# Performance work log

Hardware: AMD Instinct MI355X
Metric: run time of the kernel (lower is better)

Reference implementation:

```python
import jax, jax.numpy as jnp
import numpy as np

N_BINS = 15


def setup_inputs() -> dict:
    key = jax.random.key(0)
    k1, k2 = jax.random.split(key)
    N, C = 1000000, 100
    logits = jax.random.normal(k1, (N, C), dtype=jnp.float32)
    labels = jax.random.randint(k2, (N,), 0, C, dtype=jnp.int64)
    return {"logits": logits, "labels": labels, "t_opt": 0}


def reference(logits, labels, t_opt):
    # temperature scaling branch (t_opt is a static Python int)
    scaled = logits / t_opt if t_opt != 0 else logits
    probs = jax.nn.softmax(scaled, axis=-1)            # [N, C]
    confidences = jnp.max(probs, axis=1)               # [N]
    predictions = jnp.argmax(probs, axis=1)            # [N]
    accuracies = (predictions == labels).astype(jnp.float32)

    # bin index: confidences in (bin_lower, bin_upper] -> single-pass histogram
    boundaries = jnp.linspace(0.0, 1.0, N_BINS + 1)
    bin_idx = jnp.clip(
        jnp.searchsorted(boundaries, confidences, side="left") - 1, 0, N_BINS - 1
    )

    ones = jnp.ones_like(confidences)
    counts = jax.ops.segment_sum(ones, bin_idx, num_segments=N_BINS)
    sum_conf = jax.ops.segment_sum(confidences, bin_idx, num_segments=N_BINS)
    sum_acc = jax.ops.segment_sum(accuracies, bin_idx, num_segments=N_BINS)

    n = confidences.shape[0]
    safe = jnp.maximum(counts, 1.0)
    avg_conf = sum_conf / safe
    avg_acc = sum_acc / safe
    prop = counts / n
    per_bin = jnp.where(counts > 0, jnp.abs(avg_conf - avg_acc) * prop, 0.0)
    return jnp.sum(per_bin).reshape(1)
```

## Files before the change

kernel.cpp:

```cpp
#include <hip/hip_runtime.h>
#include <math.h>

#define NBINS 15
#define TILE_ROWS 128
#define NC 100
#define BLOCK 256
#define TILE_BYTES (TILE_ROWS * NC * 4)
#define CHUNKS (TILE_BYTES / 1024)

typedef __attribute__((address_space(3))) unsigned int lds_u32;
typedef __attribute__((address_space(1))) const unsigned int glob_u32;

__global__ __launch_bounds__(BLOCK, 3) void ece_main(const float* __restrict__ logits,
                                                     const int* __restrict__ labels,
                                                     const int* __restrict__ t_opt,
                                                     float* __restrict__ gbins,
                                                     int N) {
    __shared__ float s_tile[TILE_ROWS * NC];
    __shared__ float s_cnt[NBINS], s_conf[NBINS], s_acc[NBINS];

    const int tid  = threadIdx.x;
    if (tid < NBINS) { s_cnt[tid] = 0.f; s_conf[tid] = 0.f; s_acc[tid] = 0.f; }

    const int lane = tid & 63;
    const int wv   = tid >> 6;
    const int r    = tid >> 1;
    const int h    = tid & 1;

    const int t = t_opt[0];
    const float scale = (t != 0) ? (1.0f / (float)t) : 1.0f;
    const int nTiles = (N + TILE_ROWS - 1) / TILE_ROWS;

    for (int tile = blockIdx.x; tile < nTiles; tile += gridDim.x) {
        const long long base = (long long)tile * TILE_ROWS;
        const int rowsHere  = min(TILE_ROWS, (int)(N - base));
        const int bytesHere = rowsHere * (NC * 4);
        const char* gsrc = (const char*)(logits + base * NC);

        __syncthreads();

        #pragma unroll
        for (int i = 0; i < 13; ++i) {
            const int c = wv + i * 4;
            if (c < CHUNKS) {
                const int off = c * 1024 + lane * 16;
                if (off < bytesHere) {
                    __builtin_amdgcn_global_load_lds(
                        (glob_u32*)(gsrc + off),
                        (lds_u32*)((char*)s_tile + c * 1024),
                        16, 0, 0);
                }
            }
        }
        __syncthreads();

        if (base + r < N) {
            const float4* rowp = (const float4*)&s_tile[r * NC];
            const int n4 = 13 - h;

            float4 v[13];
            #pragma unroll
            for (int j = 0; j < 13; ++j)
                if (j < n4) v[j] = rowp[h * 13 + j];

            float m = -INFINITY; int mi = 0;
            #pragma unroll
            for (int j = 0; j < 13; ++j) if (j < n4) {
                const int cb = (h * 13 + j) * 4;
                float4 w = v[j];
                w.x *= scale; w.y *= scale; w.z *= scale; w.w *= scale;
                v[j] = w;
                if (w.x > m) { m = w.x; mi = cb;     }
                if (w.y > m) { m = w.y; mi = cb + 1; }
                if (w.z > m) { m = w.z; mi = cb + 2; }
                if (w.w > m) { m = w.w; mi = cb + 3; }
            }
            const float om  = __shfl_xor(m, 1);
            const int   omi = __shfl_xor(mi, 1);
            if (om > m || (om == m && omi < mi)) { m = om; mi = omi; }

            float e = 0.f;
            #pragma unroll
            for (int j = 0; j < 13; ++j) if (j < n4) {
                const float4 w = v[j];
                e += __expf(w.x - m) + __expf(w.y - m)
                   + __expf(w.z - m) + __expf(w.w - m);
            }
            e += __shfl_xor(e, 1);

            if (h == 0) {
                const float conf = 1.0f / e;
                const float acc  = (mi == labels[base + r]) ? 1.0f : 0.0f;

                int jc = 0;
                #pragma unroll
                for (int i = 0; i <= NBINS; ++i) {
                    const float b = (float)i * (1.0f / 15.0f);
                    jc += (b < conf) ? 1 : 0;
                }
                int bin = jc - 1;
                bin = bin < 0 ? 0 : (bin > NBINS - 1 ? NBINS - 1 : bin);

                atomicAdd(&s_cnt[bin],  1.0f);
                atomicAdd(&s_conf[bin], conf);
                atomicAdd(&s_acc[bin],  acc);
            }
        }
    }

    __syncthreads();
    if (tid < NBINS) {
        atomicAdd(&gbins[tid],             s_cnt[tid]);
        atomicAdd(&gbins[NBINS + tid],     s_conf[tid]);
        atomicAdd(&gbins[2 * NBINS + tid], s_acc[tid]);
    }
}

__global__ void ece_final(const float* __restrict__ gbins,
                          float* __restrict__ out, int N) {
    if (threadIdx.x == 0 && blockIdx.x == 0) {
        float ece = 0.f;
        for (int b = 0; b < NBINS; ++b) {
            const float c = gbins[b];
            if (c > 0.f) {
                const float avg_conf = gbins[NBINS + b] / c;
                const float avg_acc  = gbins[2 * NBINS + b] / c;
                ece += fabsf(avg_conf - avg_acc) * (c / (float)N);
            }
        }
        out[0] = ece;
    }
}

extern "C" void kernel_launch(void* const* d_in, const int* in_sizes, int n_in,
                              void* d_out, int out_size, void* d_ws, size_t ws_size,
                              hipStream_t stream) {
    const float* logits = (const float*)d_in[0];
    const int*   labels = (const int*)d_in[1];
    const int*   t_opt  = (const int*)d_in[2];
    float* out   = (float*)d_out;
    float* gbins = (float*)d_ws;

    const int N = in_sizes[1];

    hipMemsetAsync(gbins, 0, 3 * NBINS * sizeof(float), stream);

    const int nTiles = (N + TILE_ROWS - 1) / TILE_ROWS;
    const int blocks = nTiles < 768 ? nTiles : 768;
    ece_main<<<blocks, BLOCK, 0, stream>>>(logits, labels, t_opt, gbins, N);
    ece_final<<<1, 64, 0, stream>>>(gbins, out, N);
}
```

Measured before the change: 96.12 us.

## Double-buffer logits tiles in LDS with async prefetch and 4 threads per row

```diff
diff --git a/kernel.cpp b/kernel.cpp
--- a/kernel.cpp
+++ b/kernel.cpp
@@ -2,21 +2,22 @@
 #include <math.h>
 
 #define NBINS 15
-#define TILE_ROWS 128
+#define TROWS 128
 #define NC 100
-#define BLOCK 256
-#define TILE_BYTES (TILE_ROWS * NC * 4)
-#define CHUNKS (TILE_BYTES / 1024)
+#define BLOCK 512
+#define TILE_BYTES (TROWS * NC * 4)
+#define NCHUNK (TILE_BYTES / 1024)
 
 typedef __attribute__((address_space(3))) unsigned int lds_u32;
 typedef __attribute__((address_space(1))) const unsigned int glob_u32;
 
-__global__ __launch_bounds__(BLOCK, 3) void ece_main(const float* __restrict__ logits,
+__global__ __launch_bounds__(BLOCK, 2) void ece_main(const float* __restrict__ logits,
                                                      const int* __restrict__ labels,
                                                      const int* __restrict__ t_opt,
                                                      float* __restrict__ gbins,
                                                      int N) {
-    __shared__ float s_tile[TILE_ROWS * NC];
+    __shared__ float s_tile[2][TROWS * NC];
+    __shared__ int   s_lab[2][TROWS];
     __shared__ float s_cnt[NBINS], s_conf[NBINS], s_acc[NBINS];
 
     const int tid  = threadIdx.x;
@@ -24,49 +25,79 @@
 
     const int lane = tid & 63;
     const int wv   = tid >> 6;
-    const int r    = tid >> 1;
-    const int h    = tid & 1;
+    const int r    = tid >> 2;
+    const int q    = tid & 3;
 
-    const int t = t_opt[0];
-    const float scale = (t != 0) ? (1.0f / (float)t) : 1.0f;
-    const int nTiles = (N + TILE_ROWS - 1) / TILE_ROWS;
+    const int tt = t_opt[0];
+    float scale = (tt != 0) ? (1.0f / (float)tt) : 1.0f;
+    asm volatile("" :: "v"(scale));
 
-    for (int tile = blockIdx.x; tile < nTiles; tile += gridDim.x) {
-        const long long base = (long long)tile * TILE_ROWS;
-        const int rowsHere  = min(TILE_ROWS, (int)(N - base));
+    const int nTiles = (N + TROWS - 1) / TROWS;
+    const int stride = gridDim.x;
+
+    const int cstart = wv * 6 + (wv < 2 ? wv : 2);
+    const int cn     = 6 + (wv < 2 ? 1 : 0);
+
+    auto STAGE = [&](int buf, int tile) {
+        const long long rbase = (long long)tile * TROWS;
+        const int rowsHere  = min(TROWS, (int)(N - rbase));
         const int bytesHere = rowsHere * (NC * 4);
-        const char* gsrc = (const char*)(logits + base * NC);
-
-        __syncthreads();
-
+        const char* gsrc = (const char*)(logits + rbase * NC);
         #pragma unroll
-        for (int i = 0; i < 13; ++i) {
-            const int c = wv + i * 4;
-            if (c < CHUNKS) {
-                const int off = c * 1024 + lane * 16;
-                if (off < bytesHere) {
-                    __builtin_amdgcn_global_load_lds(
-                        (glob_u32*)(gsrc + off),
-                        (lds_u32*)((char*)s_tile + c * 1024),
-                        16, 0, 0);
-                }
+        for (int i = 0; i < 7; ++i) {
+            if (i < cn) {
+                const int c   = cstart + i;
+                int off = c * 1024 + lane * 16;
+                off = off < bytesHere ? off : bytesHere - 16;
+                __builtin_amdgcn_global_load_lds(
+                    (glob_u32*)(gsrc + off),
+                    (lds_u32*)((char*)&s_tile[buf][0] + c * 1024),
+                    16, 0, 0);
             }
         }
-        __syncthreads();
+        if (wv == 2 || wv == 3) {
+            int li = (wv - 2) * 64 + lane;
+            li = li < rowsHere ? li : rowsHere - 1;
+            __builtin_amdgcn_global_load_lds(
+                (glob_u32*)(labels + rbase + li),
+                (lds_u32*)&s_lab[buf][(wv - 2) * 64],
+                4, 0, 0);
+        }
+    };
 
-        if (base + r < N) {
-            const float4* rowp = (const float4*)&s_tile[r * NC];
-            const int n4 = 13 - h;
+    int cur = 0;
+    if (blockIdx.x < nTiles) STAGE(0, blockIdx.x);
 
-            float4 v[13];
+    for (int t0 = blockIdx.x; t0 < nTiles; t0 += stride) {
+        const int nxt = t0 + stride;
+        const bool hasNext = nxt < nTiles;
+        if (hasNext) STAGE(cur ^ 1, nxt);
+
+        if (hasNext) {
+            if (wv < 4) asm volatile("s_waitcnt vmcnt(7)" ::: "memory");
+            else        asm volatile("s_waitcnt vmcnt(6)" ::: "memory");
+        } else {
+            asm volatile("s_waitcnt vmcnt(0)" ::: "memory");
+        }
+        __builtin_amdgcn_sched_barrier(0);
+        __builtin_amdgcn_s_barrier();
+        __builtin_amdgcn_sched_barrier(0);
+
+        const long long rbase = (long long)t0 * TROWS;
+        if (rbase + r < N) {
+            const float4* rowp = (const float4*)&s_tile[cur][r * NC];
+            const int nf = (q == 0) ? 7 : 6;
+            const int fb = (q == 0) ? 0 : (1 + q * 6);
+
+            float4 v[7];
             #pragma unroll
-            for (int j = 0; j < 13; ++j)
-                if (j < n4) v[j] = rowp[h * 13 + j];
+            for (int j = 0; j < 7; ++j)
+                if (j < nf) v[j] = rowp[fb + j];
 
             float m = -INFINITY; int mi = 0;
             #pragma unroll
-            for (int j = 0; j < 13; ++j) if (j < n4) {
-                const int cb = (h * 13 + j) * 4;
+            for (int j = 0; j < 7; ++j) if (j < nf) {
+                const int cb = (fb + j) * 4;
                 float4 w = v[j];
                 w.x *= scale; w.y *= scale; w.z *= scale; w.w *= scale;
                 v[j] = w;
@@ -75,22 +106,26 @@
                 if (w.z > m) { m = w.z; mi = cb + 2; }
                 if (w.w > m) { m = w.w; mi = cb + 3; }
             }
-            const float om  = __shfl_xor(m, 1);
-            const int   omi = __shfl_xor(mi, 1);
-            if (om > m || (om == m && omi < mi)) { m = om; mi = omi; }
+            #pragma unroll
+            for (int off = 1; off <= 2; off <<= 1) {
+                const float om  = __shfl_xor(m, off);
+                const int   omi = __shfl_xor(mi, off);
+                if (om > m || (om == m && omi < mi)) { m = om; mi = omi; }
+            }
 
             float e = 0.f;
             #pragma unroll
-            for (int j = 0; j < 13; ++j) if (j < n4) {
+            for (int j = 0; j < 7; ++j) if (j < nf) {
                 const float4 w = v[j];
                 e += __expf(w.x - m) + __expf(w.y - m)
                    + __expf(w.z - m) + __expf(w.w - m);
             }
             e += __shfl_xor(e, 1);
+            e += __shfl_xor(e, 2);
 
-            if (h == 0) {
+            if (q == 0) {
                 const float conf = 1.0f / e;
-                const float acc  = (mi == labels[base + r]) ? 1.0f : 0.0f;
+                const float acc  = (mi == s_lab[cur][r]) ? 1.0f : 0.0f;
 
                 int jc = 0;
                 #pragma unroll
@@ -106,9 +141,18 @@
                 atomicAdd(&s_acc[bin],  acc);
             }
         }
+
+        __builtin_amdgcn_sched_barrier(0);
+        __builtin_amdgcn_s_barrier();
+        __builtin_amdgcn_sched_barrier(0);
+        cur ^= 1;
     }
 
-    __syncthreads();
+    asm volatile("s_waitcnt lgkmcnt(0)" ::: "memory");
+    __builtin_amdgcn_sched_barrier(0);
+    __builtin_amdgcn_s_barrier();
+    __builtin_amdgcn_sched_barrier(0);
+
     if (tid < NBINS) {
         atomicAdd(&gbins[tid],             s_cnt[tid]);
         atomicAdd(&gbins[NBINS + tid],     s_conf[tid]);
@@ -145,8 +189,8 @@
 
     hipMemsetAsync(gbins, 0, 3 * NBINS * sizeof(float), stream);
 
-    const int nTiles = (N + TILE_ROWS - 1) / TILE_ROWS;
-    const int blocks = nTiles < 768 ? nTiles : 768;
+    const int nTiles = (N + TROWS - 1) / TROWS;
+    const int blocks = nTiles < 256 ? nTiles : 256;
     ece_main<<<blocks, BLOCK, 0, stream>>>(logits, labels, t_opt, gbins, N);
     ece_final<<<1, 64, 0, stream>>>(gbins, out, N);
 }
```

Result: slower. 113.3 us (+17.9%).

## Prefetch next tile into registers while computing current tile from LDS

Applied to the files above, without the earlier changes.

```diff
diff --git a/kernel.cpp b/kernel.cpp
--- a/kernel.cpp
+++ b/kernel.cpp
@@ -2,71 +2,76 @@
 #include <math.h>
 
 #define NBINS 15
-#define TILE_ROWS 128
+#define TROWS 64
 #define NC 100
 #define BLOCK 256
-#define TILE_BYTES (TILE_ROWS * NC * 4)
-#define CHUNKS (TILE_BYTES / 1024)
 
-typedef __attribute__((address_space(3))) unsigned int lds_u32;
-typedef __attribute__((address_space(1))) const unsigned int glob_u32;
-
-__global__ __launch_bounds__(BLOCK, 3) void ece_main(const float* __restrict__ logits,
+__global__ __launch_bounds__(BLOCK, 4) void ece_main(const float* __restrict__ logits,
                                                      const int* __restrict__ labels,
                                                      const int* __restrict__ t_opt,
                                                      float* __restrict__ gbins,
                                                      int N) {
-    __shared__ float s_tile[TILE_ROWS * NC];
+    __shared__ __align__(16) float s_tile[TROWS * NC];
     __shared__ float s_cnt[NBINS], s_conf[NBINS], s_acc[NBINS];
 
-    const int tid  = threadIdx.x;
+    const int tid = threadIdx.x;
     if (tid < NBINS) { s_cnt[tid] = 0.f; s_conf[tid] = 0.f; s_acc[tid] = 0.f; }
 
-    const int lane = tid & 63;
-    const int wv   = tid >> 6;
-    const int r    = tid >> 1;
-    const int h    = tid & 1;
+    const int r = tid >> 2;
+    const int q = tid & 3;
 
-    const int t = t_opt[0];
-    const float scale = (t != 0) ? (1.0f / (float)t) : 1.0f;
-    const int nTiles = (N + TILE_ROWS - 1) / TILE_ROWS;
+    const int tt = t_opt[0];
+    const float scale = (tt != 0) ? (1.0f / (float)tt) : 1.0f;
 
-    for (int tile = blockIdx.x; tile < nTiles; tile += gridDim.x) {
-        const long long base = (long long)tile * TILE_ROWS;
-        const int rowsHere  = min(TILE_ROWS, (int)(N - base));
-        const int bytesHere = rowsHere * (NC * 4);
-        const char* gsrc = (const char*)(logits + base * NC);
+    const int nTiles = (N + TROWS - 1) / TROWS;
+    const int stride = gridDim.x;
 
+    float4 sv[7];
+    int    svn = 0;
+
+    auto LOADREG = [&](int tile) {
+        const long long rbase = (long long)tile * TROWS;
+        const int nf4 = min(TROWS, (int)(N - rbase)) * (NC / 4);
+        const float4* __restrict__ src = (const float4*)(logits + rbase * NC);
+        #pragma unroll
+        for (int i = 0; i < 7; ++i) {
+            const int k = tid + i * BLOCK;
+            if (k < nf4) sv[i] = src[k];
+        }
+        svn = nf4;
+    };
+
+    int t = blockIdx.x;
+    if (t < nTiles) LOADREG(t);
+
+    for (; t < nTiles; t += stride) {
         __syncthreads();
 
         #pragma unroll
-        for (int i = 0; i < 13; ++i) {
-            const int c = wv + i * 4;
-            if (c < CHUNKS) {
-                const int off = c * 1024 + lane * 16;
-                if (off < bytesHere) {
-                    __builtin_amdgcn_global_load_lds(
-                        (glob_u32*)(gsrc + off),
-                        (lds_u32*)((char*)s_tile + c * 1024),
-                        16, 0, 0);
-                }
-            }
+        for (int i = 0; i < 7; ++i) {
+            const int k = tid + i * BLOCK;
+            if (k < svn) ((float4*)s_tile)[k] = sv[i];
         }
         __syncthreads();
 
-        if (base + r < N) {
+        const int nxt = t + stride;
+        if (nxt < nTiles) LOADREG(nxt);
+
+        const long long rbase = (long long)t * TROWS;
+        if (rbase + r < N) {
             const float4* rowp = (const float4*)&s_tile[r * NC];
-            const int n4 = 13 - h;
+            const int nf = (q == 0) ? 7 : 6;
+            const int fb = (q == 0) ? 0 : (1 + q * 6);
 
-            float4 v[13];
+            float4 v[7];
             #pragma unroll
-            for (int j = 0; j < 13; ++j)
-                if (j < n4) v[j] = rowp[h * 13 + j];
+            for (int j = 0; j < 7; ++j)
+                if (j < nf) v[j] = rowp[fb + j];
 
             float m = -INFINITY; int mi = 0;
             #pragma unroll
-            for (int j = 0; j < 13; ++j) if (j < n4) {
-                const int cb = (h * 13 + j) * 4;
+            for (int j = 0; j < 7; ++j) if (j < nf) {
+                const int cb = (fb + j) * 4;
                 float4 w = v[j];
                 w.x *= scale; w.y *= scale; w.z *= scale; w.w *= scale;
                 v[j] = w;
@@ -75,22 +80,26 @@
                 if (w.z > m) { m = w.z; mi = cb + 2; }
                 if (w.w > m) { m = w.w; mi = cb + 3; }
             }
-            const float om  = __shfl_xor(m, 1);
-            const int   omi = __shfl_xor(mi, 1);
-            if (om > m || (om == m && omi < mi)) { m = om; mi = omi; }
+            #pragma unroll
+            for (int off = 1; off <= 2; off <<= 1) {
+                const float om  = __shfl_xor(m, off);
+                const int   omi = __shfl_xor(mi, off);
+                if (om > m || (om == m && omi < mi)) { m = om; mi = omi; }
+            }
 
             float e = 0.f;
             #pragma unroll
-            for (int j = 0; j < 13; ++j) if (j < n4) {
+            for (int j = 0; j < 7; ++j) if (j < nf) {
                 const float4 w = v[j];
                 e += __expf(w.x - m) + __expf(w.y - m)
                    + __expf(w.z - m) + __expf(w.w - m);
             }
             e += __shfl_xor(e, 1);
+            e += __shfl_xor(e, 2);
 
-            if (h == 0) {
+            if (q == 0) {
                 const float conf = 1.0f / e;
-                const float acc  = (mi == labels[base + r]) ? 1.0f : 0.0f;
+                const float acc  = (mi == labels[rbase + r]) ? 1.0f : 0.0f;
 
                 int jc = 0;
                 #pragma unroll
@@ -145,8 +154,8 @@
 
     hipMemsetAsync(gbins, 0, 3 * NBINS * sizeof(float), stream);
 
-    const int nTiles = (N + TILE_ROWS - 1) / TILE_ROWS;
-    const int blocks = nTiles < 768 ? nTiles : 768;
+    const int nTiles = (N + TROWS - 1) / TROWS;
+    const int blocks = nTiles < 1024 ? nTiles : 1024;
     ece_main<<<blocks, BLOCK, 0, stream>>>(logits, labels, t_opt, gbins, N);
     ece_final<<<1, 64, 0, stream>>>(gbins, out, N);
 }
```

After: 235.8 us. 145% more time.
